# Optimization experiments

Measured on AMD Instinct MI355X. Metric: run time of the kernel, lower is better.

## Reference

```python
import jax, jax.numpy as jnp
import numpy as np

B, T, C, H = 8, 1024, 768, 12
HD = C // H  # head_dim = 64


def setup_inputs() -> dict:
    key = jax.random.key(0)
    ks = jax.random.split(key, 5)
    x = jax.random.normal(ks[0], (B, T, C), dtype=jnp.float32)
    mask = jnp.tril(jnp.ones((T, T), dtype=bool))[None, None, :, :]  # causal [1,1,T,T]
    # Dense params (flax Dense: y = x @ kernel + bias)
    W_qkv = jax.random.normal(ks[1], (C, 3 * C), dtype=jnp.float32) * (1.0 / np.sqrt(C))
    b_qkv = jnp.zeros((3 * C,), dtype=jnp.float32)
    W_proj = jax.random.normal(ks[2], (C, C), dtype=jnp.float32) * (1.0 / np.sqrt(C))
    b_proj = jnp.zeros((C,), dtype=jnp.float32)
    return {"x": x, "mask": mask, "W_qkv": W_qkv, "b_qkv": b_qkv,
            "W_proj": W_proj, "b_proj": b_proj}


def reference(x, mask, W_qkv, b_qkv, W_proj, b_proj):
    Bx, Tx, Cx = x.shape
    qkv = x @ W_qkv + b_qkv                      # [B, T, 3C]
    qkv = qkv.reshape(Bx, Tx, 3 * H, HD)
    q, k, v = jnp.array_split(qkv, 3, axis=2)    # each [B, T, H, HD]
    scale = 1.0 / jnp.sqrt(jnp.float32(HD))
    attn = jnp.einsum('bqhd,bkhd->bhqk', q, k) * scale  # [B, H, T, T]
    attn = jnp.where(mask, attn, jnp.finfo(jnp.float32).min)
    attn = jax.nn.softmax(attn, axis=-1)
    out = jnp.einsum('bhqk,bkhd->bqhd', attn, v).reshape(Bx, Tx, Cx)
    return out @ W_proj + b_proj
```

## Files before the change

### kernel.cpp

```cpp
#include <hip/hip_runtime.h>


typedef unsigned short u16;
typedef unsigned int u32;
typedef __bf16 bf16x8 __attribute__((ext_vector_type(8)));
typedef float  f32x4  __attribute__((ext_vector_type(4)));
typedef float  f32x16 __attribute__((ext_vector_type(16)));
typedef unsigned short u16x4 __attribute__((ext_vector_type(4)));
typedef unsigned short u16x8 __attribute__((ext_vector_type(8)));

#define DEV static __device__ __forceinline__

constexpr int B_ = 8, T_ = 1024, C_ = 768, H_ = 12, HD_ = 64;
constexpr int M1 = B_ * T_;
constexpr int N1 = 3 * C_;
constexpr int KD = C_;

DEV u16 f2bf(float f) {
    union { float f; unsigned u; } v; v.f = f;
    unsigned r = v.u + 0x7fffu + ((v.u >> 16) & 1u);
    return (u16)(r >> 16);
}

DEV u16 bfbits(float f) {
    __bf16 h = (__bf16)f;
    union { __bf16 h; u16 u; } v; v.h = h;
    return v.u;
}

DEV void gload16(const void* g, void* l) {
    __builtin_amdgcn_global_load_lds(
        (const __attribute__((address_space(1))) unsigned*)g,
        (__attribute__((address_space(3))) unsigned*)l, 16, 0, 0);
}

DEV float redmax16(f32x16 v) {
    float a0 = fmaxf(v[0], v[1]), a1 = fmaxf(v[2], v[3]);
    float a2 = fmaxf(v[4], v[5]), a3 = fmaxf(v[6], v[7]);
    float a4 = fmaxf(v[8], v[9]), a5 = fmaxf(v[10], v[11]);
    float a6 = fmaxf(v[12], v[13]), a7 = fmaxf(v[14], v[15]);
    float b0 = fmaxf(a0, a1), b1 = fmaxf(a2, a3);
    float b2 = fmaxf(a4, a5), b3 = fmaxf(a6, a7);
    return fmaxf(fmaxf(b0, b1), fmaxf(b2, b3));
}
DEV float redsum16(f32x16 v) {
    float a0 = v[0] + v[1], a1 = v[2] + v[3], a2 = v[4] + v[5], a3 = v[6] + v[7];
    float a4 = v[8] + v[9], a5 = v[10] + v[11], a6 = v[12] + v[13], a7 = v[14] + v[15];
    float b0 = a0 + a1, b1 = a2 + a3, b2 = a4 + a5, b3 = a6 + a7;
    return (b0 + b1) + (b2 + b3);
}


__global__ __launch_bounds__(256) void cvt_x_kern(const float* __restrict__ x,
                                                  u16* __restrict__ xb, int n8) {
    int i = blockIdx.x * 256 + threadIdx.x;
    if (i >= n8) return;
    const float4* xf = (const float4*)x;
    float4 a = xf[i * 2], b = xf[i * 2 + 1];
    u16x8 o;
    o[0] = f2bf(a.x); o[1] = f2bf(a.y); o[2] = f2bf(a.z); o[3] = f2bf(a.w);
    o[4] = f2bf(b.x); o[5] = f2bf(b.y); o[6] = f2bf(b.z); o[7] = f2bf(b.w);
    *(u16x8*)(xb + (size_t)i * 8) = o;
}

__global__ __launch_bounds__(256) void cvt_wT_kern(const float* __restrict__ W,
                                                   u16* __restrict__ Wt, int K, int N) {
    __shared__ float tile[32][33];
    int n0 = blockIdx.x * 32, k0 = blockIdx.y * 32;
    int tx = threadIdx.x & 31, ty = threadIdx.x >> 5;
#pragma unroll
    for (int i = 0; i < 4; i++) {
        int k = ty * 4 + i;
        tile[k][tx] = W[(size_t)(k0 + k) * N + n0 + tx];
    }
    __syncthreads();
#pragma unroll
    for (int i = 0; i < 4; i++) {
        int n = ty * 4 + i;
        Wt[(size_t)(n0 + n) * K + k0 + tx] = f2bf(tile[tx][n]);
    }
}


template <int MODE>
__global__ __launch_bounds__(256, 2) void gemm_bt_kern(
    const u16* __restrict__ A, const u16* __restrict__ Bt,
    const float* __restrict__ bias, int nBN,
    u16* __restrict__ qw, u16* __restrict__ kw, u16* __restrict__ vw,
    float* __restrict__ out) {
    __shared__ u16 ldsA[128 * 64];
    __shared__ u16 ldsB[128 * 64];
    const int bm = blockIdx.x / nBN, bn = blockIdx.x % nBN;
    const int m0 = bm * 128, n0 = bn * 128;
    const int t = threadIdx.x;
    const int lane = t & 63, w = t >> 6;
    const int wr = w >> 1, wc = w & 1;
    const int l15 = lane & 15, lhi = lane >> 4;
    const int srow = t >> 3;
    const int scb = ((t & 7) << 4) ^ ((srow & 7) << 4);
    const char* Ab = (const char*)(A + (size_t)(m0 + srow) * KD) + scb;
    const char* Bb = (const char*)(Bt + (size_t)(n0 + srow) * KD) + scb;
    char* lA = (char*)ldsA + w * 1024;
    char* lB = (char*)ldsB + w * 1024;

    f32x4 acc[4][4] = {};

    for (int k0 = 0; k0 < KD; k0 += 64) {
#pragma unroll
        for (int s = 0; s < 4; s++) {
            gload16(Ab + (size_t)k0 * 2 + (size_t)s * 32 * KD * 2, lA + s * 4096);
            gload16(Bb + (size_t)k0 * 2 + (size_t)s * 32 * KD * 2, lB + s * 4096);
        }
        __syncthreads();
#pragma unroll
        for (int kk = 0; kk < 2; kk++) {
            bf16x8 af[4], bfr[4];
#pragma unroll
            for (int i = 0; i < 4; i++) {
                int rowA = wr * 64 + i * 16 + l15;
                af[i] = *(const bf16x8*)((const char*)ldsA + rowA * 128 +
                                         ((kk * 64 + lhi * 16) ^ ((rowA & 7) << 4)));
                int rowB = wc * 64 + i * 16 + l15;
                bfr[i] = *(const bf16x8*)((const char*)ldsB + rowB * 128 +
                                          ((kk * 64 + lhi * 16) ^ ((rowB & 7) << 4)));
            }
#pragma unroll
            for (int fm = 0; fm < 4; fm++)
#pragma unroll
                for (int fn = 0; fn < 4; fn++)
                    acc[fm][fn] = __builtin_amdgcn_mfma_f32_16x16x32_bf16(
                        af[fm], bfr[fn], acc[fm][fn], 0, 0, 0);
        }
        __syncthreads();
    }

    if constexpr (MODE == 1) {
#pragma unroll
        for (int fm = 0; fm < 4; fm++) {
            const int mb = m0 + wr * 64 + fm * 16 + lhi * 4;
#pragma unroll
            for (int fn = 0; fn < 4; fn++) {
                const int n = n0 + wc * 64 + fn * 16 + l15;
                const float bv = bias[n];
#pragma unroll
                for (int r = 0; r < 4; r++)
                    out[(size_t)(mb + r) * C_ + n] = acc[fm][fn][r] + bv;
            }
        }
    } else {
#pragma unroll
        for (int fn = 0; fn < 4; fn++) {
            const int c0 = n0 + wc * 64 + fn * 16;
            const int h3 = c0 >> 6;
            const int d = (c0 & 63) + l15;
            const float bv = bias[c0 + l15];
#pragma unroll
            for (int fm = 0; fm < 4; fm++) {
                const int mb = m0 + wr * 64 + fm * 16 + lhi * 4;
                const int b = mb >> 10, tq = mb & 1023;
                if (h3 < H_) {
                    u16* dst = qw + ((size_t)(b * H_ + h3) * T_ + tq) * HD_ + d;
#pragma unroll
                    for (int r = 0; r < 4; r++)
                        dst[r * HD_] = f2bf((acc[fm][fn][r] + bv) * 0.125f);
                } else if (h3 < 2 * H_) {
                    u16* dst = kw + ((size_t)(b * H_ + (h3 - H_)) * T_ + tq) * HD_ + d;
#pragma unroll
                    for (int r = 0; r < 4; r++)
                        dst[r * HD_] = f2bf(acc[fm][fn][r] + bv);
                } else {
                    u16x4 p;
#pragma unroll
                    for (int r = 0; r < 4; r++) p[r] = f2bf(acc[fm][fn][r] + bv);
                    *(u16x4*)(vw + ((size_t)(b * H_ + (h3 - 2 * H_)) * HD_ + d) * T_ + tq) = p;
                }
            }
        }
    }
}


__global__ __launch_bounds__(256, 3) void attn_fwd_kern(
    const u16* __restrict__ qg, const u16* __restrict__ kg,
    const u16* __restrict__ vg, u16* __restrict__ ao) {
    __shared__ u16 kld[2][64 * 64];
    __shared__ u16 vld[2][64 * 64];
    __shared__ u16 pld[4][32 * 64];
    const int n = blockIdx.x;
    const int bh = (n & 7) + 8 * ((n >> 3) % 12);
    const int qt = 7 - n / 96;
    const int t = threadIdx.x, lane = t & 63, w = t >> 6;
    const int q5 = lane & 31, h2 = lane >> 5;
    const int srow = t >> 3;
    const int scb = ((t & 7) << 4) ^ ((srow & 7) << 4);
    const char* kb = (const char*)(kg + (size_t)bh * T_ * HD_);
    const char* vb = (const char*)(vg + (size_t)bh * HD_ * T_);

    const int qrow_g = qt * 128 + w * 32 + q5;
    const u16* qrow = qg + (size_t)bh * T_ * HD_ + (size_t)qrow_g * HD_ + h2 * 8;
    bf16x8 qf[4];
#pragma unroll
    for (int kc = 0; kc < 4; kc++)
        qf[kc] = *(const bf16x8*)(qrow + kc * 16);

#pragma unroll
    for (int s = 0; s < 2; s++) {
        gload16(kb + (size_t)(srow + s * 32) * 128 + scb,
                (char*)kld[0] + w * 1024 + s * 4096);
        gload16(vb + (size_t)(srow + s * 32) * 2048 + scb,
                (char*)vld[0] + w * 1024 + s * 4096);
    }
    __syncthreads();

    f32x16 acc[2] = {};
    float mst = -1e30f, lst = 0.f;
    const int qmax = qt * 128 + w * 32 + 31;
    char* pw = (char*)pld[w];

    const int ntiles = 2 * qt + 2;
    for (int kvt = 0; kvt < ntiles; kvt++) {
        const int cur = kvt & 1;
        if (kvt + 1 < ntiles) {
#pragma unroll
            for (int s = 0; s < 2; s++) {
                gload16(kb + (size_t)((kvt + 1) * 64 + srow + s * 32) * 128 + scb,
                        (char*)kld[cur ^ 1] + w * 1024 + s * 4096);
                gload16(vb + (size_t)(srow + s * 32) * 2048 + (kvt + 1) * 128 + scb,
                        (char*)vld[cur ^ 1] + w * 1024 + s * 4096);
            }
        }
        if (kvt * 64 <= qmax) {
            const char* kbase = (const char*)kld[cur];
            const char* vbase = (const char*)vld[cur];
            f32x16 s0 = {}, s1 = {};
            __builtin_amdgcn_s_setprio(1);
#pragma unroll
            for (int kc = 0; kc < 4; kc++) {
                const int r0 = q5, r1 = 32 + q5;
                bf16x8 kf0 = *(const bf16x8*)(kbase + r0 * 128 +
                                              ((kc * 32 + h2 * 16) ^ ((r0 & 7) << 4)));
                bf16x8 kf1 = *(const bf16x8*)(kbase + r1 * 128 +
                                              ((kc * 32 + h2 * 16) ^ ((r1 & 7) << 4)));
                s0 = __builtin_amdgcn_mfma_f32_32x32x16_bf16(kf0, qf[kc], s0, 0, 0, 0);
                s1 = __builtin_amdgcn_mfma_f32_32x32x16_bf16(kf1, qf[kc], s1, 0, 0, 0);
            }
            __builtin_amdgcn_s_setprio(0);
            if (kvt * 64 + 63 > qt * 128 + w * 32) {
                const int qg_ = qrow_g, kvb0 = kvt * 64 + 4 * h2;
#pragma unroll
                for (int r = 0; r < 16; r++) {
                    const int kvo = (r & 3) + 8 * (r >> 2);
                    if (kvb0 + kvo > qg_) s0[r] = -1e30f;
                    if (kvb0 + 32 + kvo > qg_) s1[r] = -1e30f;
                }
            }
            float pmax = fmaxf(redmax16(s0), redmax16(s1));
            pmax = fmaxf(pmax, __shfl_xor(pmax, 32));
            const float mn = fmaxf(mst, pmax);
            const float corr = __expf(mst - mn);
            mst = mn;
#pragma unroll
            for (int r = 0; r < 16; r++) {
                s0[r] = __expf(s0[r] - mn);
                s1[r] = __expf(s1[r] - mn);
            }
            float rs = redsum16(s0) + redsum16(s1);
            rs += __shfl_xor(rs, 32);
            lst = lst * corr + rs;
#pragma unroll
            for (int r = 0; r < 16; r++) { acc[0][r] *= corr; acc[1][r] *= corr; }
            const int swz = (q5 & 7) << 4;
#pragma unroll
            for (int a = 0; a < 8; a++) {
                const int kv0 = ((2 * a) & 3) + 8 * (a >> 1) + 4 * h2;
                u32 pk0 = (u32)bfbits(s0[2 * a]) | ((u32)bfbits(s0[2 * a + 1]) << 16);
                u32 pk1 = (u32)bfbits(s1[2 * a]) | ((u32)bfbits(s1[2 * a + 1]) << 16);
                *(u32*)(pw + q5 * 128 + ((kv0 * 2) ^ swz)) = pk0;
                *(u32*)(pw + q5 * 128 + (((kv0 + 32) * 2) ^ swz)) = pk1;
            }
            bf16x8 pf[4];
#pragma unroll
            for (int m = 0; m < 4; m++)
                pf[m] = *(const bf16x8*)(pw + q5 * 128 + ((m * 32 + h2 * 16) ^ swz));
            __builtin_amdgcn_s_setprio(1);
#pragma unroll
            for (int m = 0; m < 4; m++) {
#pragma unroll
                for (int db = 0; db < 2; db++) {
                    const int rd = db * 32 + q5;
                    bf16x8 vf = *(const bf16x8*)(vbase + rd * 128 +
                                                 ((m * 32 + h2 * 16) ^ ((rd & 7) << 4)));
                    acc[db] = __builtin_amdgcn_mfma_f32_32x32x16_bf16(vf, pf[m], acc[db], 0, 0, 0);
                }
            }
            __builtin_amdgcn_s_setprio(0);
        }
        __syncthreads();
    }

    const int b = bh / H_, h = bh % H_;
    const float inv = 1.0f / lst;
    u16* orow = ao + (size_t)(b * T_ + qrow_g) * C_ + h * 64 + 4 * h2;
#pragma unroll
    for (int db = 0; db < 2; db++)
#pragma unroll
        for (int q2 = 0; q2 < 4; q2++) {
            u16x4 pk;
#pragma unroll
            for (int e = 0; e < 4; e++) pk[e] = bfbits(acc[db][q2 * 4 + e] * inv);
            *(u16x4*)(orow + db * 32 + q2 * 8) = pk;
        }
}


extern "C" void kernel_launch(void* const* d_in, const int* in_sizes, int n_in,
                              void* d_out, int out_size, void* d_ws, size_t ws_size,
                              hipStream_t stream) {
    const float* x     = (const float*)d_in[0];
    const float* Wqkv  = (const float*)d_in[2];
    const float* bqkv  = (const float*)d_in[3];
    const float* Wproj = (const float*)d_in[4];
    const float* bproj = (const float*)d_in[5];
    float* out = (float*)d_out;

    char* ws = (char*)d_ws;
    u16* xb     = (u16*)(ws);
    u16* wqkvT  = (u16*)(ws + 12582912);
    u16* wprojT = (u16*)(ws + 16121856);
    u16* qw     = (u16*)(ws + 17301504);
    u16* kw     = (u16*)(ws + 29884416);
    u16* vw     = (u16*)(ws + 42467328);
    u16* ao     = (u16*)(ws + 55050240);

    cvt_x_kern<<<(M1 * C_ / 8 + 255) / 256, 256, 0, stream>>>(x, xb, M1 * C_ / 8);
    cvt_wT_kern<<<dim3(N1 / 32, KD / 32), 256, 0, stream>>>(Wqkv, wqkvT, KD, N1);
    cvt_wT_kern<<<dim3(C_ / 32, KD / 32), 256, 0, stream>>>(Wproj, wprojT, KD, C_);

    gemm_bt_kern<0><<<(M1 / 128) * (N1 / 128), 256, 0, stream>>>(
        xb, wqkvT, bqkv, N1 / 128, qw, kw, vw, nullptr);

    attn_fwd_kern<<<B_ * H_ * (T_ / 128), 256, 0, stream>>>(qw, kw, vw, ao);

    gemm_bt_kern<1><<<(M1 / 128) * (C_ / 128), 256, 0, stream>>>(
        ao, wprojT, bproj, C_ / 128, nullptr, nullptr, nullptr, out);
}
```

Before: 111.9 us.

## Double-buffer GEMM LDS tiles, add XCD block remap, merge weight conversions

The GEMM kernel now keeps two LDS buffers for A and B. It issues the global-to-LDS loads for the next K step before computing on the current one, so load latency can overlap the MFMA work. Block IDs are remapped so that consecutive tiles land on the same XCD, which should improve L2 reuse. The two weight transpose/convert launches are merged into one kernel to remove a launch. The cost is double the LDS footprint per block (64KB), which can lower occupancy.

```diff
diff --git a/kernel.cpp b/kernel.cpp
--- a/kernel.cpp
+++ b/kernel.cpp
@@ -63,10 +63,16 @@
     *(u16x8*)(xb + (size_t)i * 8) = o;
 }
 
-__global__ __launch_bounds__(256) void cvt_wT_kern(const float* __restrict__ W,
-                                                   u16* __restrict__ Wt, int K, int N) {
+__global__ __launch_bounds__(256) void cvt_w_kern(const float* __restrict__ Wq,
+                                                  const float* __restrict__ Wp,
+                                                  u16* __restrict__ WqT,
+                                                  u16* __restrict__ WpT) {
     __shared__ float tile[32][33];
-    int n0 = blockIdx.x * 32, k0 = blockIdx.y * 32;
+    int bx = blockIdx.x;
+    const float* W; u16* Wt; int N;
+    if (bx < N1 / 32) { W = Wq; Wt = WqT; N = N1; }
+    else { bx -= N1 / 32; W = Wp; Wt = WpT; N = C_; }
+    int n0 = bx * 32, k0 = blockIdx.y * 32;
     int tx = threadIdx.x & 31, ty = threadIdx.x >> 5;
 #pragma unroll
     for (int i = 0; i < 4; i++) {
@@ -77,7 +83,7 @@
 #pragma unroll
     for (int i = 0; i < 4; i++) {
         int n = ty * 4 + i;
-        Wt[(size_t)(n0 + n) * K + k0 + tx] = f2bf(tile[tx][n]);
+        Wt[(size_t)(n0 + n) * KD + k0 + tx] = f2bf(tile[tx][n]);
     }
 }
 
@@ -88,9 +94,11 @@
     const float* __restrict__ bias, int nBN,
     u16* __restrict__ qw, u16* __restrict__ kw, u16* __restrict__ vw,
     float* __restrict__ out) {
-    __shared__ u16 ldsA[128 * 64];
-    __shared__ u16 ldsB[128 * 64];
-    const int bm = blockIdx.x / nBN, bn = blockIdx.x % nBN;
+    __shared__ u16 ldsA[2][128 * 64];
+    __shared__ u16 ldsB[2][128 * 64];
+    const int cpx = gridDim.x >> 3;
+    const int bid = (blockIdx.x & 7) * cpx + (blockIdx.x >> 3);
+    const int bm = bid / nBN, bn = bid % nBN;
     const int m0 = bm * 128, n0 = bn * 128;
     const int t = threadIdx.x;
     const int lane = t & 63, w = t >> 6;
@@ -100,28 +108,37 @@
     const int scb = ((t & 7) << 4) ^ ((srow & 7) << 4);
     const char* Ab = (const char*)(A + (size_t)(m0 + srow) * KD) + scb;
     const char* Bb = (const char*)(Bt + (size_t)(n0 + srow) * KD) + scb;
-    char* lA = (char*)ldsA + w * 1024;
-    char* lB = (char*)ldsB + w * 1024;
-
-    f32x4 acc[4][4] = {};
-
-    for (int k0 = 0; k0 < KD; k0 += 64) {
+
+    auto stage = [&](int buf, int k0) {
+        char* lA = (char*)ldsA[buf] + w * 1024;
+        char* lB = (char*)ldsB[buf] + w * 1024;
 #pragma unroll
         for (int s = 0; s < 4; s++) {
             gload16(Ab + (size_t)k0 * 2 + (size_t)s * 32 * KD * 2, lA + s * 4096);
             gload16(Bb + (size_t)k0 * 2 + (size_t)s * 32 * KD * 2, lB + s * 4096);
         }
-        __syncthreads();
+    };
+
+    stage(0, 0);
+    __syncthreads();
+
+    f32x4 acc[4][4] = {};
+    constexpr int NSTEP = KD / 64;
+    for (int st = 0; st < NSTEP; ++st) {
+        const int cur = st & 1;
+        if (st + 1 < NSTEP) stage(cur ^ 1, (st + 1) * 64);
+        const char* baseA = (const char*)ldsA[cur];
+        const char* baseB = (const char*)ldsB[cur];
 #pragma unroll
         for (int kk = 0; kk < 2; kk++) {
             bf16x8 af[4], bfr[4];
 #pragma unroll
             for (int i = 0; i < 4; i++) {
                 int rowA = wr * 64 + i * 16 + l15;
-                af[i] = *(const bf16x8*)((const char*)ldsA + rowA * 128 +
+                af[i] = *(const bf16x8*)(baseA + rowA * 128 +
                                          ((kk * 64 + lhi * 16) ^ ((rowA & 7) << 4)));
                 int rowB = wc * 64 + i * 16 + l15;
-                bfr[i] = *(const bf16x8*)((const char*)ldsB + rowB * 128 +
+                bfr[i] = *(const bf16x8*)(baseB + rowB * 128 +
                                           ((kk * 64 + lhi * 16) ^ ((rowB & 7) << 4)));
             }
 #pragma unroll
@@ -333,8 +350,8 @@
     u16* ao     = (u16*)(ws + 55050240);
 
     cvt_x_kern<<<(M1 * C_ / 8 + 255) / 256, 256, 0, stream>>>(x, xb, M1 * C_ / 8);
-    cvt_wT_kern<<<dim3(N1 / 32, KD / 32), 256, 0, stream>>>(Wqkv, wqkvT, KD, N1);
-    cvt_wT_kern<<<dim3(C_ / 32, KD / 32), 256, 0, stream>>>(Wproj, wprojT, KD, C_);
+    cvt_w_kern<<<dim3(N1 / 32 + C_ / 32, KD / 32), 256, 0, stream>>>(
+        Wqkv, Wproj, wqkvT, wprojT);
 
     gemm_bt_kern<0><<<(M1 / 128) * (N1 / 128), 256, 0, stream>>>(
         xb, wqkvT, bqkv, N1 / 128, qw, kw, vw, nullptr);
```

Result: no change. 114.1 us (+1.9%).
